# Kernel tuning notes

Measured on AMD Instinct MI355X. Metric: run time of the kernel, lower is better.

Reference implementation:

```python
import jax, jax.numpy as jnp
import numpy as np

B, G, T, N = 4, 8, 30, 60
CT, CN = 1, 60
FD, IDD = 256, 256
E = FD + IDD          # 512
H = 8                 # (FD+IDD)//head_dim
L = 6                 # num_layers
VP1 = 51              # num_id_vocabulary + 1
PE = 32               # rel_pe_length
DFF = 4 * E


def _ln(x, g, b, eps=1e-5):
    m = x.mean(-1, keepdims=True)
    v = ((x - m) ** 2).mean(-1, keepdims=True)
    return (x - m) / jnp.sqrt(v + eps) * g + b


def _mha(qx, kx, vx, Wqkv, bqkv, Wo, bo, bias, h):
    # torch nn.MultiheadAttention with add_zero_attn=True; bias is additive
    # attn bias of shape [B, h, Lq, Lk+1] (already padded for the zero-attn col).
    e = qx.shape[-1]
    d = e // h
    Wq, Wk, Wv = jnp.split(Wqkv, 3, axis=0)
    bq, bk, bv = jnp.split(bqkv, 3)
    q = qx @ Wq.T + bq
    k = kx @ Wk.T + bk
    v = vx @ Wv.T + bv
    b_, lq, _ = q.shape
    lk = k.shape[1]
    z = jnp.zeros((b_, 1, e), q.dtype)
    k = jnp.concatenate([k, z], axis=1)   # add_zero_attn appends zero key
    v = jnp.concatenate([v, z], axis=1)
    qh = q.reshape(b_, lq, h, d).transpose(0, 2, 1, 3)
    kh = k.reshape(b_, lk + 1, h, d).transpose(0, 2, 1, 3)
    vh = v.reshape(b_, lk + 1, h, d).transpose(0, 2, 1, 3)
    s = jnp.einsum('bhqd,bhkd->bhqk', qh, kh) / jnp.sqrt(jnp.float32(d)) + bias
    p = jax.nn.softmax(s, axis=-1)
    o = jnp.einsum('bhqk,bhkd->bhqd', p, vh).transpose(0, 2, 1, 3).reshape(b_, lq, e)
    return o @ Wo.T + bo


def _forward(tf, uf, ids, tt_, ut_, tm, um, Ww, Wout, rpe,
             saW, sab, saO, saob, sag, sabn,
             caW, cab, caO, caob, cag, cabn,
             f1, fb1, f2, fb2, fg, fbn):
    b, g, t, n, fd = tf.shape
    _, _, ct, cn, _ = uf.shape
    id_dim = Ww.shape[0]
    e = fd + id_dim
    nl = caW.shape[0]
    h = rpe.shape[-1]
    pe = rpe.shape[1]
    # one_hot(label) @ W_word.T == W_word[:, label]
    traj_id = Ww.T[ids]                                        # b g t n id
    unk_id = jnp.broadcast_to(Ww[:, VP1 - 1], (b, g, ct, cn, id_dim))
    traj = jnp.concatenate([tf, traj_id], -1).reshape(b * g, t * n, e)
    unk = jnp.concatenate([uf, unk_id], -1)                    # b g ct cn e

    tt = tt_.reshape(b * g, t * n)
    ut = ut_.reshape(b * g, ct * cn)
    neg = jnp.float32(-jnp.inf)
    zero = jnp.float32(0)
    causal = jnp.where(tt[:, None, :] >= ut[:, :, None], neg, zero)  # bg q k
    kpm = jnp.where(tm.reshape(b * g, t * n), neg, zero)             # bg k
    # torch rel_pos_map[u, t] = u - t; negative torch indices wrap -> mod pe
    rel_idx = (ut[:, :, None] - tt[:, None, :]) % pe                 # bg q k
    sa_bias = jnp.pad(
        jnp.where(um.reshape(b * g * ct, cn), neg, zero)[:, None, None, :],
        ((0, 0), (0, 0), (0, 0), (0, 1)))

    for l in range(nl):
        if l > 0:
            x = unk.reshape(b * g * ct, cn, e)
            y = _mha(x, x, x, saW[l - 1], sab[l - 1], saO[l - 1], saob[l - 1], sa_bias, h)
            unk = _ln(x + y, sag[l - 1], sabn[l - 1]).reshape(b, g, ct, cn, e)
        q = unk.reshape(b * g, ct * cn, e)
        rel = rpe[l][rel_idx]                                  # bg q k h  (gathered rel-PE)
        bias = causal[:, None] + jnp.transpose(rel, (0, 3, 1, 2)) + kpm[:, None, None, :]
        bias = jnp.pad(bias, ((0, 0), (0, 0), (0, 0), (0, 1)))
        y = _mha(q, traj, traj, caW[l], cab[l], caO[l], caob[l], bias, h)
        x = _ln(q + y, cag[l], cabn[l])
        hh = jax.nn.gelu(x @ f1[l].T + fb1[l], approximate=False) @ f2[l].T + fb2[l]
        x = _ln(x + hh, fg[l], fbn[l])
        unk = x.reshape(b, g, ct, cn, e)
    # final layer logits (eval mode): shared embed_to_word head, no bias
    return unk[..., fd:] @ Wout.T


def setup_inputs():
    key = jax.random.key(0)
    ks = iter(jax.random.split(key, 48))
    nrm = lambda shape, s=0.02: jax.random.normal(next(ks), shape, jnp.float32) * s
    return {
        'trajectory_features': jax.random.normal(next(ks), (B, G, T, N, FD), jnp.float32),
        'unknown_features': jax.random.normal(next(ks), (B, G, CT, CN, FD), jnp.float32),
        'trajectory_id_labels': jax.random.randint(next(ks), (B, G, T, N), 0, VP1),
        'trajectory_times': jax.random.randint(next(ks), (B, G, T, N), 0, PE),
        'unknown_times': jax.random.randint(next(ks), (B, G, CT, CN), 0, PE),
        'trajectory_masks': jnp.zeros((B, G, T, N), bool),
        'unknown_masks': jnp.zeros((B, G, CT, CN), bool),
        'use_decoder_checkpoint': 0,
        'W_word': nrm((IDD, VP1), 0.05),
        'W_out': nrm((VP1, IDD), 0.05),
        'rel_pos_embeds': nrm((L, PE, H), 0.1),
        'sa_Wqkv': nrm((L - 1, 3 * E, E)), 'sa_bqkv': jnp.zeros((L - 1, 3 * E)),
        'sa_Wo': nrm((L - 1, E, E)), 'sa_bo': jnp.zeros((L - 1, E)),
        'sa_ln_g': jnp.ones((L - 1, E)), 'sa_ln_b': jnp.zeros((L - 1, E)),
        'ca_Wqkv': nrm((L, 3 * E, E)), 'ca_bqkv': jnp.zeros((L, 3 * E)),
        'ca_Wo': nrm((L, E, E)), 'ca_bo': jnp.zeros((L, E)),
        'ca_ln_g': jnp.ones((L, E)), 'ca_ln_b': jnp.zeros((L, E)),
        'ffn_W1': nrm((L, DFF, E)), 'ffn_b1': jnp.zeros((L, DFF)),
        'ffn_W2': nrm((L, E, DFF)), 'ffn_b2': jnp.zeros((L, E)),
        'ffn_ln_g': jnp.ones((L, E)), 'ffn_ln_b': jnp.zeros((L, E)),
    }


def reference(trajectory_features, unknown_features, trajectory_id_labels,
              trajectory_times, unknown_times, trajectory_masks, unknown_masks,
              use_decoder_checkpoint, W_word, W_out, rel_pos_embeds,
              sa_Wqkv, sa_bqkv, sa_Wo, sa_bo, sa_ln_g, sa_ln_b,
              ca_Wqkv, ca_bqkv, ca_Wo, ca_bo, ca_ln_g, ca_ln_b,
              ffn_W1, ffn_b1, ffn_W2, ffn_b2, ffn_ln_g, ffn_ln_b):
    return _forward(trajectory_features, unknown_features, trajectory_id_labels,
                    trajectory_times, unknown_times, trajectory_masks, unknown_masks,
                    W_word, W_out, rel_pos_embeds,
                    sa_Wqkv, sa_bqkv, sa_Wo, sa_bo, sa_ln_g, sa_ln_b,
                    ca_Wqkv, ca_bqkv, ca_Wo, ca_bo, ca_ln_g, ca_ln_b,
                    ffn_W1, ffn_b1, ffn_W2, ffn_b2, ffn_ln_g, ffn_ln_b)
```

## Files before the change

kernel.cpp:

```cpp
#include <hip/hip_runtime.h>
#include <cmath>

__device__ __forceinline__ float bflo(unsigned int u) {
  union { unsigned int i; float f; } v; v.i = u << 16; return v.f;
}
__device__ __forceinline__ float bfhi(unsigned int u) {
  union { unsigned int i; float f; } v; v.i = u & 0xffff0000u; return v.f;
}
__device__ __forceinline__ float bf2f(unsigned short u) {
  union { unsigned int i; float f; } v; v.i = ((unsigned int)u) << 16; return v.f;
}
__device__ __forceinline__ unsigned short f2bf(float f) {
  union { float f; unsigned int i; } v; v.f = f;
  unsigned int i = v.i;
  return (unsigned short)((i + 0x7fffu + ((i >> 16) & 1u)) >> 16);
}

typedef __attribute__((ext_vector_type(8))) short short8;
typedef __attribute__((ext_vector_type(4))) float floatx4;

__global__ __launch_bounds__(256) void conv_kernel(
    const float* __restrict__ in, unsigned short* __restrict__ out, int n)
{
  int i = (blockIdx.x * 256 + threadIdx.x) << 2;
  if (i >= n) return;
  float4 v = *reinterpret_cast<const float4*>(in + i);
  ushort4 o;
  o.x = f2bf(v.x); o.y = f2bf(v.y); o.z = f2bf(v.z); o.w = f2bf(v.w);
  *reinterpret_cast<ushort4*>(out + i) = o;
}

__global__ __launch_bounds__(256) void gemm_mfma(
    const unsigned short* __restrict__ A, int lda,
    const unsigned short* __restrict__ W, int ldw,
    const float* __restrict__ bias,
    void* __restrict__ Cv, int ldc,
    int K, int act, int cbf16, int swz)
{
  __shared__ __align__(16) unsigned short As[128 * 32];
  __shared__ __align__(16) unsigned short Bs[128 * 32];
  const int tid = threadIdx.x;
  const int wave = tid >> 6, lane = tid & 63;

  int bxi = blockIdx.x, byi = blockIdx.y;
  if (swz) {
    int f = byi * gridDim.x + bxi;
    int q = (gridDim.x * gridDim.y) >> 3;
    f = (f & 7) * q + (f >> 3);
    bxi = f % gridDim.x;
    byi = f / gridDim.x;
  }
  const int bm = byi * 128, bn = bxi * 128;
  const int wm = (wave >> 1) << 6, wn = (wave & 1) << 6;

  floatx4 acc[4][4];
#pragma unroll
  for (int i = 0; i < 4; ++i)
#pragma unroll
    for (int j = 0; j < 4; ++j) acc[i][j] = (floatx4){0.f, 0.f, 0.f, 0.f};

  const int srow = (wave << 5) + (lane >> 2);
  const int scol = (lane & 3) << 3;
  const unsigned short* Ag  = A + (size_t)(bm + srow) * lda + scol;
  const unsigned short* Wg  = W + (size_t)(bn + srow) * ldw + scol;
  const unsigned short* Ag2 = Ag + (size_t)16 * lda;
  const unsigned short* Wg2 = Wg + (size_t)16 * ldw;
  unsigned short* AsW = As + (wave << 5) * 32;
  unsigned short* BsW = Bs + (wave << 5) * 32;

  const unsigned short* a_rd = As + (size_t)(wm + (lane & 15)) * 32 + ((lane >> 4) << 3);
  const unsigned short* b_rd = Bs + (size_t)(wn + (lane & 15)) * 32 + ((lane >> 4) << 3);

  for (int k0 = 0; k0 < K; k0 += 32) {
    __builtin_amdgcn_global_load_lds(
        (const __attribute__((address_space(1))) unsigned int*)(Ag + k0),
        (__attribute__((address_space(3))) unsigned int*)(AsW), 16, 0, 0);
    __builtin_amdgcn_global_load_lds(
        (const __attribute__((address_space(1))) unsigned int*)(Ag2 + k0),
        (__attribute__((address_space(3))) unsigned int*)(AsW + 16 * 32), 16, 0, 0);
    __builtin_amdgcn_global_load_lds(
        (const __attribute__((address_space(1))) unsigned int*)(Wg + k0),
        (__attribute__((address_space(3))) unsigned int*)(BsW), 16, 0, 0);
    __builtin_amdgcn_global_load_lds(
        (const __attribute__((address_space(1))) unsigned int*)(Wg2 + k0),
        (__attribute__((address_space(3))) unsigned int*)(BsW + 16 * 32), 16, 0, 0);
    __syncthreads();
    short8 af[4], bf[4];
#pragma unroll
    for (int i = 0; i < 4; ++i) {
      af[i] = *reinterpret_cast<const short8*>(a_rd + (size_t)(i << 4) * 32);
      bf[i] = *reinterpret_cast<const short8*>(b_rd + (size_t)(i << 4) * 32);
    }
#pragma unroll
    for (int i = 0; i < 4; ++i)
#pragma unroll
      for (int j = 0; j < 4; ++j)
        acc[i][j] = __builtin_amdgcn_mfma_f32_16x16x32_bf16(af[i], bf[j], acc[i][j], 0, 0, 0);
    __syncthreads();
  }

  const int col0 = lane & 15;
  const int row0 = (lane >> 4) << 2;
#pragma unroll
  for (int i = 0; i < 4; ++i) {
#pragma unroll
    for (int j = 0; j < 4; ++j) {
      int col = bn + wn + (j << 4) + col0;
      float bv = bias ? bias[col] : 0.f;
#pragma unroll
      for (int r = 0; r < 4; ++r) {
        int row = bm + wm + (i << 4) + row0 + r;
        float v = acc[i][j][r] + bv;
        if (act) v = 0.5f * v * (1.f + erff(v * 0.70710678f));
        if (cbf16) ((unsigned short*)Cv)[(size_t)row * ldc + col] = f2bf(v);
        else       ((float*)Cv)[(size_t)row * ldc + col] = v;
      }
    }
  }
}

__device__ __forceinline__ float wred_max(float v) {
#pragma unroll
  for (int off = 32; off > 0; off >>= 1) v = fmaxf(v, __shfl_xor(v, off, 64));
  return v;
}
__device__ __forceinline__ float wred_sum(float v) {
#pragma unroll
  for (int off = 32; off > 0; off >>= 1) v += __shfl_xor(v, off, 64);
  return v;
}

#define LDK 72
__global__ __launch_bounds__(512) void attn_mfma_kernel(
    const unsigned short* __restrict__ Qp,
    const unsigned short* __restrict__ KVb,
    unsigned short* __restrict__ O,
    const int* __restrict__ tt, const int* __restrict__ ut,
    const unsigned char* __restrict__ km,
    const float* __restrict__ rel)
{
  const int bg = blockIdx.x >> 3, h = blockIdx.x & 7;
  const int tid = threadIdx.x;
  const int grp = tid >> 8;
  const int wave = (tid >> 6) & 3;
  const int lane = tid & 63;
  const int quad = lane >> 4, mrow = lane & 15;

  __shared__ __align__(16) unsigned short SMEM[6 * 64 * LDK];
  unsigned short* Ks = SMEM + grp * (3 * 64 * LDK);
  unsigned short* Vt = Ks + 64 * LDK;
  unsigned short* Ps = Vt + 64 * LDK;

  const int qa = wave * 16 + mrow;
  const int qc = qa < 60 ? qa : 59;
  const unsigned short* qptr = Qp + (size_t)(bg * 60 + qc) * 512 + h * 64 + quad * 8;
  const short8 af0 = *reinterpret_cast<const short8*>(qptr);
  const short8 af1 = *reinterpret_cast<const short8*>(qptr + 32);

  const float relreg = rel[(lane & 31) * 8 + h];

  int tq[4];
  float m[4], l[4];
  floatx4 acc[4];
#pragma unroll
  for (int r = 0; r < 4; ++r) {
    int qo = wave * 16 + quad * 4 + r;
    tq[r] = ut[bg * 60 + (qo < 60 ? qo : 59)];
    m[r] = grp ? -1e30f : 0.f;
    l[r] = grp ? 0.f : 1.f;
  }
#pragma unroll
  for (int nt = 0; nt < 4; ++nt) acc[nt] = (floatx4){0.f, 0.f, 0.f, 0.f};

  const int sk = tid & 255;
  const int stok = sk >> 2, schk = sk & 3;

  for (int it = 0; it < 15; ++it) {
    const int k0 = (grp + 2 * it) << 6;
    __syncthreads();
    {
      const int key = k0 + stok;
      uint4 kr0 = {0,0,0,0}, kr1 = {0,0,0,0}, vr0 = {0,0,0,0}, vr1 = {0,0,0,0};
      if (key < 1800) {
        const unsigned short* kb = KVb + ((size_t)bg * 1800 + key) * 1024 + h * 64 + schk * 16;
        kr0 = *reinterpret_cast<const uint4*>(kb);
        kr1 = *reinterpret_cast<const uint4*>(kb + 8);
        vr0 = *reinterpret_cast<const uint4*>(kb + 512);
        vr1 = *reinterpret_cast<const uint4*>(kb + 520);
      }
      *reinterpret_cast<uint4*>(&Ks[stok * LDK + schk * 16]) = kr0;
      *reinterpret_cast<uint4*>(&Ks[stok * LDK + schk * 16 + 8]) = kr1;
      unsigned int wv[8] = {vr0.x, vr0.y, vr0.z, vr0.w, vr1.x, vr1.y, vr1.z, vr1.w};
#pragma unroll
      for (int e = 0; e < 16; ++e)
        Vt[(schk * 16 + e) * LDK + stok] = (unsigned short)(wv[e >> 1] >> ((e & 1) * 16));
    }
    int meta = 0x10000;
    {
      int kk = k0 + lane;
      if (kk < 1800) {
        int base = bg * 1800 + kk;
        meta = tt[base] | (km[base] ? 0x10000 : 0);
      }
    }
    __syncthreads();

    floatx4 S[4];
#pragma unroll
    for (int nt = 0; nt < 4; ++nt) {
      const unsigned short* kb = Ks + (nt * 16 + mrow) * LDK + quad * 8;
      short8 b0 = *reinterpret_cast<const short8*>(kb);
      short8 b1 = *reinterpret_cast<const short8*>(kb + 32);
      floatx4 s = (floatx4){0.f, 0.f, 0.f, 0.f};
      s = __builtin_amdgcn_mfma_f32_16x16x32_bf16(af0, b0, s, 0, 0, 0);
      s = __builtin_amdgcn_mfma_f32_16x16x32_bf16(af1, b1, s, 0, 0, 0);
      S[nt] = s;
    }
    int mcol[4];
#pragma unroll
    for (int nt = 0; nt < 4; ++nt)
      mcol[nt] = __builtin_amdgcn_ds_bpermute((nt * 16 + mrow) << 2, meta);
    float sv[4][4];
#pragma unroll
    for (int nt = 0; nt < 4; ++nt) {
      int tk = mcol[nt] & 0xffff;
      int bad0 = mcol[nt] >> 16;
#pragma unroll
      for (int r = 0; r < 4; ++r) {
        float v = S[nt][r] * 0.125f;
        int ridx = (tq[r] - tk) & 31;
        v += __int_as_float(__builtin_amdgcn_ds_bpermute(ridx << 2, __float_as_int(relreg)));
        sv[nt][r] = (bad0 | (tk >= tq[r])) ? -1e30f : v;
      }
    }
#pragma unroll
    for (int r = 0; r < 4; ++r) {
      float rm = fmaxf(fmaxf(sv[0][r], sv[1][r]), fmaxf(sv[2][r], sv[3][r]));
#pragma unroll
      for (int d = 1; d < 16; d <<= 1) rm = fmaxf(rm, __shfl_xor(rm, d, 64));
      float nm = fmaxf(m[r], rm);
      float corr = __expf(m[r] - nm);
      float ps = 0.f;
      const int prow = (wave * 16 + quad * 4 + r) * LDK + mrow;
#pragma unroll
      for (int nt = 0; nt < 4; ++nt) {
        float p = __expf(sv[nt][r] - nm);
        ps += p;
        Ps[prow + nt * 16] = f2bf(p);
      }
#pragma unroll
      for (int d = 1; d < 16; d <<= 1) ps += __shfl_xor(ps, d, 64);
      l[r] = l[r] * corr + ps;
      m[r] = nm;
#pragma unroll
      for (int nt = 0; nt < 4; ++nt) acc[nt][r] *= corr;
    }
    const unsigned short* pp = Ps + (wave * 16 + mrow) * LDK + quad * 8;
    short8 a0 = *reinterpret_cast<const short8*>(pp);
    short8 a1 = *reinterpret_cast<const short8*>(pp + 32);
#pragma unroll
    for (int nt = 0; nt < 4; ++nt) {
      const unsigned short* vb = Vt + (nt * 16 + mrow) * LDK + quad * 8;
      short8 b0 = *reinterpret_cast<const short8*>(vb);
      short8 b1 = *reinterpret_cast<const short8*>(vb + 32);
      acc[nt] = __builtin_amdgcn_mfma_f32_16x16x32_bf16(a0, b0, acc[nt], 0, 0, 0);
      acc[nt] = __builtin_amdgcn_mfma_f32_16x16x32_bf16(a1, b1, acc[nt], 0, 0, 0);
    }
  }

  __syncthreads();
  float* MA = (float*)SMEM;
  float* Ml = (float*)(SMEM + 64 * 68 * 2);
  float* Ll = Ml + 64;
  if (grp == 1) {
#pragma unroll
    for (int r = 0; r < 4; ++r) {
      int row = wave * 16 + quad * 4 + r;
#pragma unroll
      for (int nt = 0; nt < 4; ++nt)
        MA[row * 68 + nt * 16 + mrow] = acc[nt][r];
      if (mrow == 0) { Ml[row] = m[r]; Ll[row] = l[r]; }
    }
  }
  __syncthreads();
  if (grp == 0) {
#pragma unroll
    for (int r = 0; r < 4; ++r) {
      int row = wave * 16 + quad * 4 + r;
      float m1 = Ml[row], l1 = Ll[row];
      float M = fmaxf(m[r], m1);
      float c0 = __expf(m[r] - M), c1 = __expf(m1 - M);
      float invL = 1.f / (l[r] * c0 + l1 * c1);
      if (row < 60) {
        unsigned short* op = O + (size_t)(bg * 60 + row) * 512 + h * 64;
#pragma unroll
        for (int nt = 0; nt < 4; ++nt) {
          float o = (acc[nt][r] * c0 + MA[row * 68 + nt * 16 + mrow] * c1) * invL;
          op[nt * 16 + mrow] = f2bf(o);
        }
      }
    }
  }
}

#define QPB 32
#define QPW 8
__global__ __launch_bounds__(256) void attn2_kernel(
    const unsigned short* __restrict__ Qp, int qs,
    const unsigned short* __restrict__ Kp, int ks,
    const unsigned short* __restrict__ Vp, int vs,
    unsigned short* __restrict__ O, int os, int kLen,
    const unsigned char* __restrict__ kmask)
{
  const int bg = blockIdx.x >> 3;
  const int h  = blockIdx.x & 7;
  const int q0 = blockIdx.y * QPB;
  const int tid = threadIdx.x;
  const int wave = tid >> 6, lane = tid & 63;

  __shared__ float Qs[QPB][68];
  __shared__ float Ks[64][68];
  __shared__ float Vs[64][68];
  __shared__ float Ps[QPB][68];

  {
    int qr = tid >> 3, j = tid & 7;
    int q = q0 + qr;
    float f[8] = {0, 0, 0, 0, 0, 0, 0, 0};
    if (q < 60) {
      uint4 v = *reinterpret_cast<const uint4*>(Qp + (size_t)(bg * 60 + q) * qs + h * 64 + j * 8);
      f[0] = bflo(v.x); f[1] = bfhi(v.x); f[2] = bflo(v.y); f[3] = bfhi(v.y);
      f[4] = bflo(v.z); f[5] = bfhi(v.z); f[6] = bflo(v.w); f[7] = bfhi(v.w);
    }
#pragma unroll
    for (int e = 0; e < 8; ++e) Qs[qr][j * 8 + e] = f[e];
  }

  float m[QPW], l[QPW], acc[QPW];
#pragma unroll
  for (int i = 0; i < QPW; ++i) { m[i] = 0.f; l[i] = 1.f; acc[i] = 0.f; }

  const int std = tid >> 2;
  const int stj = tid & 3;

  for (int k0 = 0; k0 < kLen; k0 += 64) {
    __syncthreads();
    const bool sok = (k0 + std) < kLen;
    {
      const unsigned short* kb = Kp + ((size_t)bg * kLen + k0 + std) * ks + h * 64 + stj * 16;
      float f[16];
#pragma unroll
      for (int e = 0; e < 16; ++e) f[e] = 0.f;
      if (sok) {
        uint4 v0 = *reinterpret_cast<const uint4*>(kb);
        uint4 v1 = *reinterpret_cast<const uint4*>(kb + 8);
        f[0] = bflo(v0.x); f[1] = bfhi(v0.x); f[2]  = bflo(v0.y); f[3]  = bfhi(v0.y);
        f[4] = bflo(v0.z); f[5] = bfhi(v0.z); f[6]  = bflo(v0.w); f[7]  = bfhi(v0.w);
        f[8] = bflo(v1.x); f[9] = bfhi(v1.x); f[10] = bflo(v1.y); f[11] = bfhi(v1.y);
        f[12] = bflo(v1.z); f[13] = bfhi(v1.z); f[14] = bflo(v1.w); f[15] = bfhi(v1.w);
      }
#pragma unroll
      for (int e = 0; e < 16; ++e) Ks[stj * 16 + e][std] = f[e];
    }
    {
      const unsigned short* vb = Vp + ((size_t)bg * kLen + k0 + std) * vs + h * 64;
#pragma unroll
      for (int c = 0; c < 2; ++c) {
        int off = c * 32 + stj * 8;
        float f[8] = {0, 0, 0, 0, 0, 0, 0, 0};
        if (sok) {
          uint4 v = *reinterpret_cast<const uint4*>(vb + off);
          f[0] = bflo(v.x); f[1] = bfhi(v.x); f[2] = bflo(v.y); f[3] = bfhi(v.y);
          f[4] = bflo(v.z); f[5] = bfhi(v.z); f[6] = bflo(v.w); f[7] = bfhi(v.w);
        }
#pragma unroll
        for (int e = 0; e < 8; ++e) Vs[std][off + e] = f[e];
      }
    }
    const int kk = k0 + lane;
    const bool kok = kk < kLen;
    unsigned char kmv = 0;
    if (kok && kmask) kmv = kmask[(size_t)bg * kLen + kk];
    __syncthreads();

    float s[QPW];
#pragma unroll
    for (int i = 0; i < QPW; ++i) s[i] = 0.f;
    for (int d = 0; d < 64; ++d) {
      float kv = Ks[d][lane];
#pragma unroll
      for (int i = 0; i < QPW; ++i)
        s[i] = fmaf(Qs[wave * QPW + i][d], kv, s[i]);
    }

    const int kmax = min(64, kLen - k0);
#pragma unroll
    for (int i = 0; i < QPW; ++i) {
      float svv = s[i] * 0.125f;
      if (kmv || !kok) svv = -1e30f;
      float nm = fmaxf(m[i], wred_max(svv));
      float p = __expf(svv - nm);
      float ts = wred_sum(p);
      float corr = __expf(m[i] - nm);
      l[i] = l[i] * corr + ts;
      acc[i] *= corr;
      m[i] = nm;
      Ps[wave * QPW + i][lane] = p;
    }
    for (int k = 0; k < kmax; ++k) {
      float v = Vs[k][lane];
#pragma unroll
      for (int i = 0; i < QPW; ++i)
        acc[i] = fmaf(Ps[wave * QPW + i][k], v, acc[i]);
    }
  }

#pragma unroll
  for (int i = 0; i < QPW; ++i) {
    int q = q0 + wave * QPW + i;
    if (q < 60)
      O[(size_t)(bg * 60 + q) * os + h * 64 + lane] = f2bf(acc[i] / l[i]);
  }
}

__global__ __launch_bounds__(256) void add_ln_kernel(
    const float* __restrict__ a, const float* __restrict__ b,
    const float* __restrict__ g, const float* __restrict__ be,
    float* __restrict__ o, unsigned short* __restrict__ ob)
{
  const int t = blockIdx.x;
  const int tid = threadIdx.x;
  const int wave = tid >> 6, lane = tid & 63;
  const size_t base = (size_t)t * 512;
  float v0 = a[base + tid] + b[base + tid];
  float v1 = a[base + 256 + tid] + b[base + 256 + tid];
  __shared__ float red[4];
  float s = wred_sum(v0 + v1);
  if (lane == 0) red[wave] = s;
  __syncthreads();
  float mean = (red[0] + red[1] + red[2] + red[3]) * (1.0f / 512.0f);
  float d0 = v0 - mean, d1 = v1 - mean;
  float vs = wred_sum(d0 * d0 + d1 * d1);
  __syncthreads();
  if (lane == 0) red[wave] = vs;
  __syncthreads();
  float var = (red[0] + red[1] + red[2] + red[3]) * (1.0f / 512.0f);
  float rstd = rsqrtf(var + 1e-5f);
  float r0 = d0 * rstd * g[tid] + be[tid];
  float r1 = d1 * rstd * g[256 + tid] + be[256 + tid];
  o[base + tid] = r0;
  o[base + 256 + tid] = r1;
  ob[base + tid] = f2bf(r0);
  ob[base + 256 + tid] = f2bf(r1);
}

__global__ __launch_bounds__(256) void build_traj_kernel(
    const float* __restrict__ tf, const int* __restrict__ ids,
    const float* __restrict__ Ww, unsigned short* __restrict__ traj)
{
  int idx = blockIdx.x * 256 + threadIdx.x;
  int tok = idx >> 9;
  int j = idx & 511;
  float v = (j < 256) ? tf[((size_t)tok << 8) + j] : Ww[(j - 256) * 51 + ids[tok]];
  traj[idx] = f2bf(v);
}

__global__ __launch_bounds__(256) void build_unk_kernel(
    const float* __restrict__ uf, const float* __restrict__ Ww,
    float* __restrict__ x, unsigned short* __restrict__ xb)
{
  int idx = blockIdx.x * 256 + threadIdx.x;
  int tok = idx >> 9;
  int j = idx & 511;
  float v = (j < 256) ? uf[((size_t)tok << 8) + j] : Ww[(j - 256) * 51 + 50];
  x[idx] = v;
  xb[idx] = f2bf(v);
}

__global__ __launch_bounds__(64) void head_kernel(
    const float* __restrict__ x, const float* __restrict__ Wout, float* __restrict__ out)
{
  const int t = blockIdx.x;
  const int tid = threadIdx.x;
  __shared__ float xs[256];
  for (int i = tid; i < 256; i += 64) xs[i] = x[(size_t)t * 512 + 256 + i];
  __syncthreads();
  if (tid < 51) {
    const float* w = Wout + tid * 256;
    float s = 0.f;
    for (int k = 0; k < 256; ++k) s = fmaf(xs[k], w[k], s);
    out[t * 51 + tid] = s;
  }
}

extern "C" void kernel_launch(void* const* d_in, const int* in_sizes, int n_in,
                              void* d_out, int out_size, void* d_ws, size_t ws_size,
                              hipStream_t stream) {
  const float* tf  = (const float*)d_in[0];
  const float* uf  = (const float*)d_in[1];
  const int*   ids = (const int*)d_in[2];
  const int*   tt  = (const int*)d_in[3];
  const int*   ut  = (const int*)d_in[4];
  const unsigned char* tm = (const unsigned char*)d_in[5];
  const unsigned char* um = (const unsigned char*)d_in[6];
  const float* Ww   = (const float*)d_in[8];
  const float* Wout = (const float*)d_in[9];
  const float* rpe  = (const float*)d_in[10];
  const float* saW  = (const float*)d_in[11];
  const float* sab  = (const float*)d_in[12];
  const float* saO  = (const float*)d_in[13];
  const float* saob = (const float*)d_in[14];
  const float* sag  = (const float*)d_in[15];
  const float* sabn = (const float*)d_in[16];
  const float* caW  = (const float*)d_in[17];
  const float* cab  = (const float*)d_in[18];
  const float* caO  = (const float*)d_in[19];
  const float* caob = (const float*)d_in[20];
  const float* cag  = (const float*)d_in[21];
  const float* cabn = (const float*)d_in[22];
  const float* f1   = (const float*)d_in[23];
  const float* fb1  = (const float*)d_in[24];
  const float* f2   = (const float*)d_in[25];
  const float* fb2  = (const float*)d_in[26];
  const float* fg   = (const float*)d_in[27];
  const float* fbn  = (const float*)d_in[28];

  unsigned short* trajb = (unsigned short*)d_ws;
  unsigned short* KVb   = trajb + (size_t)29491200;
  unsigned short* qkvb  = KVb   + (size_t)58982400;
  unsigned short* hb    = qkvb  + (size_t)2949120;
  unsigned short* xb    = hb    + (size_t)3932160;
  float* x    = (float*)(xb + (size_t)983040);
  float* ybuf = x + (size_t)983040;
  unsigned short* wtail = (unsigned short*)(ybuf + (size_t)983040);

  const size_t NEED = (size_t)200540160 + (size_t)24117248 * 2;
  const bool pre = ws_size >= NEED;
  unsigned short* wsa  = wtail;
  unsigned short* wsaO = wsa  + (size_t)3932160;
  unsigned short* wca  = wsaO + (size_t)1310720;
  unsigned short* wcaO = wca  + (size_t)4718592;
  unsigned short* wf1  = wcaO + (size_t)1572864;
  unsigned short* wf2  = wf1  + (size_t)6291456;
  unsigned short* wconv = wtail;

  if (pre) {
    conv_kernel<<<dim3(3840), dim3(256), 0, stream>>>(saW, wsa, 3932160);
    conv_kernel<<<dim3(1280), dim3(256), 0, stream>>>(saO, wsaO, 1310720);
    conv_kernel<<<dim3(4608), dim3(256), 0, stream>>>(caW, wca, 4718592);
    conv_kernel<<<dim3(1536), dim3(256), 0, stream>>>(caO, wcaO, 1572864);
    conv_kernel<<<dim3(6144), dim3(256), 0, stream>>>(f1, wf1, 6291456);
    conv_kernel<<<dim3(6144), dim3(256), 0, stream>>>(f2, wf2, 6291456);
  }

  build_traj_kernel<<<dim3(115200), dim3(256), 0, stream>>>(tf, ids, Ww, trajb);
  build_unk_kernel<<<dim3(3840), dim3(256), 0, stream>>>(uf, Ww, x, xb);

  for (int l = 0; l < 6; ++l) {
    if (l > 0) {
      int sl = l - 1;
      const unsigned short* wq;
      if (pre) wq = wsa + (size_t)sl * 786432;
      else {
        conv_kernel<<<dim3(768), dim3(256), 0, stream>>>(saW + (size_t)sl * 786432, wconv, 786432);
        wq = wconv;
      }
      gemm_mfma<<<dim3(12, 15), dim3(256), 0, stream>>>(
          xb, 512, wq, 512, sab + sl * 1536, qkvb, 1536, 512, 0, 1, 0);
      attn2_kernel<<<dim3(256, 2), dim3(256), 0, stream>>>(
          qkvb, 1536, qkvb + 512, 1536, qkvb + 1024, 1536, hb, 512, 60, um);
      const unsigned short* wo;
      if (pre) wo = wsaO + (size_t)sl * 262144;
      else {
        conv_kernel<<<dim3(256), dim3(256), 0, stream>>>(saO + (size_t)sl * 262144, wconv, 262144);
        wo = wconv;
      }
      gemm_mfma<<<dim3(4, 15), dim3(256), 0, stream>>>(
          hb, 512, wo, 512, saob + sl * 512, ybuf, 512, 512, 0, 0, 0);
      add_ln_kernel<<<dim3(1920), dim3(256), 0, stream>>>(x, ybuf, sag + sl * 512, sabn + sl * 512, x, xb);
    }
    const unsigned short* wqkv;
    if (pre) wqkv = wca + (size_t)l * 786432;
    else {
      conv_kernel<<<dim3(768), dim3(256), 0, stream>>>(caW + (size_t)l * 786432, wconv, 786432);
      wqkv = wconv;
    }
    gemm_mfma<<<dim3(8, 450), dim3(256), 0, stream>>>(
        trajb, 512, wqkv + 262144, 512, cab + l * 1536 + 512, KVb, 1024, 512, 0, 1, 1);
    gemm_mfma<<<dim3(4, 15), dim3(256), 0, stream>>>(
        xb, 512, wqkv, 512, cab + l * 1536, qkvb, 512, 512, 0, 1, 0);
    attn_mfma_kernel<<<dim3(256), dim3(512), 0, stream>>>(
        qkvb, KVb, hb, tt, ut, tm, rpe + l * 256);
    const unsigned short* wco;
    if (pre) wco = wcaO + (size_t)l * 262144;
    else {
      conv_kernel<<<dim3(256), dim3(256), 0, stream>>>(caO + (size_t)l * 262144, wconv, 262144);
      wco = wconv;
    }
    gemm_mfma<<<dim3(4, 15), dim3(256), 0, stream>>>(
        hb, 512, wco, 512, caob + l * 512, ybuf, 512, 512, 0, 0, 0);
    add_ln_kernel<<<dim3(1920), dim3(256), 0, stream>>>(x, ybuf, cag + l * 512, cabn + l * 512, x, xb);
    const unsigned short* w1;
    if (pre) w1 = wf1 + (size_t)l * 1048576;
    else {
      conv_kernel<<<dim3(1024), dim3(256), 0, stream>>>(f1 + (size_t)l * 1048576, wconv, 1048576);
      w1 = wconv;
    }
    gemm_mfma<<<dim3(16, 15), dim3(256), 0, stream>>>(
        xb, 512, w1, 512, fb1 + l * 2048, hb, 2048, 512, 1, 1, 0);
    const unsigned short* w2;
    if (pre) w2 = wf2 + (size_t)l * 1048576;
    else {
      conv_kernel<<<dim3(1024), dim3(256), 0, stream>>>(f2 + (size_t)l * 1048576, wconv, 1048576);
      w2 = wconv;
    }
    gemm_mfma<<<dim3(4, 15), dim3(256), 0, stream>>>(
        hb, 2048, w2, 2048, fb2 + l * 512, ybuf, 512, 2048, 0, 0, 0);
    add_ln_kernel<<<dim3(1920), dim3(256), 0, stream>>>(x, ybuf, fg + l * 512, fbn + l * 512, x, xb);
  }
  head_kernel<<<dim3(1920), dim3(64), 0, stream>>>(x, Wout, (float*)d_out);
}
```

Before: 2.211 ms.

## Double-buffer GEMM LDS tiles and XOR-swizzle layout to avoid bank conflicts

Restructures the MFMA GEMM main loop so it keeps two LDS buffers. The load for tile t+2 is issued right after the current tile's fragments are read into registers, so global-to-LDS transfers overlap the MFMA work. Explicit vmcnt/lgkmcnt waits and barriers replace the __syncthreads calls. It also XOR-swizzles the 16-byte chunk column by row, on both the global load side and the LDS read side, to reduce LDS bank conflicts. In exchange, LDS use per block doubles, which may lower occupancy, and the hand-written wait counts must match the number of outstanding loads.

```diff
diff --git a/kernel.cpp b/kernel.cpp
--- a/kernel.cpp
+++ b/kernel.cpp
@@ -37,8 +37,8 @@
     void* __restrict__ Cv, int ldc,
     int K, int act, int cbf16, int swz)
 {
-  __shared__ __align__(16) unsigned short As[128 * 32];
-  __shared__ __align__(16) unsigned short Bs[128 * 32];
+  __shared__ __align__(16) unsigned short As[2][128 * 32];
+  __shared__ __align__(16) unsigned short Bs[2][128 * 32];
   const int tid = threadIdx.x;
   const int wave = tid >> 6, lane = tid & 63;
 
@@ -60,44 +60,64 @@
     for (int j = 0; j < 4; ++j) acc[i][j] = (floatx4){0.f, 0.f, 0.f, 0.f};
 
   const int srow = (wave << 5) + (lane >> 2);
-  const int scol = (lane & 3) << 3;
+  const int chsw = (lane & 3) ^ ((srow >> 1) & 3);
+  const int scol = chsw << 3;
   const unsigned short* Ag  = A + (size_t)(bm + srow) * lda + scol;
   const unsigned short* Wg  = W + (size_t)(bn + srow) * ldw + scol;
   const unsigned short* Ag2 = Ag + (size_t)16 * lda;
   const unsigned short* Wg2 = Wg + (size_t)16 * ldw;
-  unsigned short* AsW = As + (wave << 5) * 32;
-  unsigned short* BsW = Bs + (wave << 5) * 32;
-
-  const unsigned short* a_rd = As + (size_t)(wm + (lane & 15)) * 32 + ((lane >> 4) << 3);
-  const unsigned short* b_rd = Bs + (size_t)(wn + (lane & 15)) * 32 + ((lane >> 4) << 3);
-
-  for (int k0 = 0; k0 < K; k0 += 32) {
-    __builtin_amdgcn_global_load_lds(
-        (const __attribute__((address_space(1))) unsigned int*)(Ag + k0),
-        (__attribute__((address_space(3))) unsigned int*)(AsW), 16, 0, 0);
-    __builtin_amdgcn_global_load_lds(
-        (const __attribute__((address_space(1))) unsigned int*)(Ag2 + k0),
-        (__attribute__((address_space(3))) unsigned int*)(AsW + 16 * 32), 16, 0, 0);
-    __builtin_amdgcn_global_load_lds(
-        (const __attribute__((address_space(1))) unsigned int*)(Wg + k0),
-        (__attribute__((address_space(3))) unsigned int*)(BsW), 16, 0, 0);
-    __builtin_amdgcn_global_load_lds(
-        (const __attribute__((address_space(1))) unsigned int*)(Wg2 + k0),
-        (__attribute__((address_space(3))) unsigned int*)(BsW + 16 * 32), 16, 0, 0);
-    __syncthreads();
+  const int ldsw = (wave << 5) * 32;
+
+  const int arow = lane & 15;
+  const int rsw  = (arow >> 1) & 3;
+  const int chrd = (lane >> 4) ^ rsw;
+  const int aoff = (wm + arow) * 32 + (chrd << 3);
+  const int boff = (wn + arow) * 32 + (chrd << 3);
+
+  const int nt = K >> 5;
+
+#define STAGE(b, t)                                                                 \
+  do {                                                                              \
+    const int k0_ = (t) << 5;                                                       \
+    __builtin_amdgcn_global_load_lds(                                               \
+        (const __attribute__((address_space(1))) unsigned int*)(Ag + k0_),          \
+        (__attribute__((address_space(3))) unsigned int*)(As[(b)] + ldsw), 16, 0, 0); \
+    __builtin_amdgcn_global_load_lds(                                               \
+        (const __attribute__((address_space(1))) unsigned int*)(Ag2 + k0_),         \
+        (__attribute__((address_space(3))) unsigned int*)(As[(b)] + ldsw + 16 * 32), 16, 0, 0); \
+    __builtin_amdgcn_global_load_lds(                                               \
+        (const __attribute__((address_space(1))) unsigned int*)(Wg + k0_),          \
+        (__attribute__((address_space(3))) unsigned int*)(Bs[(b)] + ldsw), 16, 0, 0); \
+    __builtin_amdgcn_global_load_lds(                                               \
+        (const __attribute__((address_space(1))) unsigned int*)(Wg2 + k0_),         \
+        (__attribute__((address_space(3))) unsigned int*)(Bs[(b)] + ldsw + 16 * 32), 16, 0, 0); \
+  } while (0)
+
+  STAGE(0, 0);
+  if (nt > 1) STAGE(1, 1);
+
+  int cur = 0;
+  for (int t = 0; t < nt; ++t) {
+    if (t + 1 < nt) asm volatile("s_waitcnt vmcnt(4)\n\ts_barrier" ::: "memory");
+    else            asm volatile("s_waitcnt vmcnt(0)\n\ts_barrier" ::: "memory");
+
     short8 af[4], bf[4];
 #pragma unroll
     for (int i = 0; i < 4; ++i) {
-      af[i] = *reinterpret_cast<const short8*>(a_rd + (size_t)(i << 4) * 32);
-      bf[i] = *reinterpret_cast<const short8*>(b_rd + (size_t)(i << 4) * 32);
-    }
+      af[i] = *reinterpret_cast<const short8*>(&As[cur][aoff + (i << 4) * 32]);
+      bf[i] = *reinterpret_cast<const short8*>(&Bs[cur][boff + (i << 4) * 32]);
+    }
+    asm volatile("s_waitcnt lgkmcnt(0)\n\ts_barrier" ::: "memory");
+    if (t + 2 < nt) STAGE(cur, t + 2);
+
 #pragma unroll
     for (int i = 0; i < 4; ++i)
 #pragma unroll
       for (int j = 0; j < 4; ++j)
         acc[i][j] = __builtin_amdgcn_mfma_f32_16x16x32_bf16(af[i], bf[j], acc[i][j], 0, 0, 0);
-    __syncthreads();
-  }
+    cur ^= 1;
+  }
+#undef STAGE
 
   const int col0 = lane & 15;
   const int row0 = (lane >> 4) << 2;
```

Measured after the change: 1.995 ms. 9.8% less time.
